# Kernel tuning notes

Hardware: AMD Instinct MI355X
Metric: run time of the kernel (lower is better)

The kernel has to match this reference:

```python
import jax, jax.numpy as jnp
import numpy as np

RES = 0.1
TABLE = 2 ** 20
MOD_T = 201
HEADS = 8
M = 500_000
D = 120
PRIMES_NP = np.array([73856093, 19349669, 83492791], dtype=np.int64)
BMIN = np.array([-2.6, -8.1, 0.0], dtype=np.float32)
BMAX = np.array([4.6, 4.7, 3.1], dtype=np.float32)
CORNERS = [(0, 0, 0), (1, 0, 0), (0, 1, 0), (0, 0, 1), (1, 1, 0), (1, 0, 1), (0, 1, 1), (1, 1, 1)]


def _build_hash_table():
    # Mirror torch.arange / meshgrid voxel grid construction.
    xs = np.arange(BMIN[0], BMAX[0], RES, dtype=np.float32)
    ys = np.arange(BMIN[1], BMAX[1], RES, dtype=np.float32)
    zs = np.arange(BMIN[2], BMAX[2], RES, dtype=np.float32)
    gx, gy, gz = np.meshgrid(xs, ys, zs, indexing='ij')
    vox = np.stack([gx, gy, gz], axis=-1).reshape(-1, 3)
    grid = np.floor(vox / RES).astype(np.int64)
    h = np.remainder((grid * PRIMES_NP).sum(-1), TABLE)
    buf = np.full(TABLE, -1, dtype=np.int64)
    uh, first_idx = np.unique(h, return_index=True)
    buf[uh] = first_idx
    return buf, vox.shape[0]


def setup_inputs() -> dict:
    key = jax.random.key(0)
    ks = jax.random.split(key, 12)
    buf_np, total_voxels = _build_hash_table()
    u = jax.random.uniform(ks[0], (M, 3), dtype=jnp.float32)
    query_pts = jnp.asarray(BMIN) + u * jnp.asarray(BMAX - BMIN)
    query_times = jax.random.randint(ks[1], (M,), 0, 1000, dtype=jnp.int64)
    dynamic_features = jax.random.normal(ks[2], (total_voxels, D), dtype=jnp.float32) * 0.01
    time_embeddings = jax.random.normal(ks[3], (MOD_T, D), dtype=jnp.float32) * 0.01
    s = 1.0 / np.sqrt(D)
    Wq = jax.random.normal(ks[4], (D, D), dtype=jnp.float32) * s
    Wk = jax.random.normal(ks[5], (D, D), dtype=jnp.float32) * s
    Wv = jax.random.normal(ks[6], (D, D), dtype=jnp.float32) * s
    Wo = jax.random.normal(ks[7], (D, D), dtype=jnp.float32) * s
    bq = jnp.zeros((D,), jnp.float32)
    bk = jnp.zeros((D,), jnp.float32)
    bv = jnp.zeros((D,), jnp.float32)
    bo = jnp.zeros((D,), jnp.float32)
    return {
        'query_pts': query_pts, 'query_times': query_times,
        'dynamic_features': dynamic_features, 'time_embeddings': time_embeddings,
        'buffer_voxel_index': jnp.asarray(buf_np),
        'Wq': Wq, 'bq': bq, 'Wk': Wk, 'bk': bk, 'Wv': Wv, 'bv': bv, 'Wo': Wo, 'bo': bo,
    }


def _attn_fuse(feat, time_emb, Wq, bq, Wk, bk, Wv, bv, Wo, bo):
    # 2-token self-attention fusion: tokens = [voxel feature, time embedding]
    m, d = feat.shape
    dh = d // HEADS
    x = jnp.stack([feat, time_emb], axis=1)  # (M, 2, D)
    q = (x @ Wq + bq).reshape(m, 2, HEADS, dh)
    k = (x @ Wk + bk).reshape(m, 2, HEADS, dh)
    v = (x @ Wv + bv).reshape(m, 2, HEADS, dh)
    scores = jnp.einsum('mqhd,mkhd->mhqk', q, k) / jnp.sqrt(jnp.float32(dh))
    a = jax.nn.softmax(scores, axis=-1)
    o = jnp.einsum('mhqk,mkhd->mqhd', a, v).reshape(m, 2, d)
    o = o @ Wo + bo
    return o.mean(axis=1)  # (M, D)


def reference(query_pts, query_times, dynamic_features, time_embeddings,
              buffer_voxel_index, Wq, bq, Wk, bk, Wv, bv, Wo, bo):
    primes = jnp.asarray(PRIMES_NP)
    m = query_pts.shape[0]
    d = dynamic_features.shape[1]
    t_mod = jnp.remainder(query_times, MOD_T)

    gf = query_pts / RES
    gfl = jnp.floor(gf)
    frac = gf - gfl                      # (M, 3)
    base = gfl.astype(jnp.int64)         # (M, 3)

    accum = jnp.zeros((m, d), dtype=query_pts.dtype)
    for ox, oy, oz in CORNERS:           # fixed structural 8-corner loop
        cc = base + jnp.asarray([ox, oy, oz], dtype=jnp.int64)
        h = jnp.remainder((cc * primes).sum(-1), TABLE)
        vidx = buffer_voxel_index[h]
        valid = vidx >= 0
        wx = frac[:, 0] if ox else 1.0 - frac[:, 0]
        wy = frac[:, 1] if oy else 1.0 - frac[:, 1]
        wz = frac[:, 2] if oz else 1.0 - frac[:, 2]
        w = wx * wy * wz                 # (M,)
        f = dynamic_features[jnp.where(valid, vidx, 0)]
        accum = accum + jnp.where(valid[:, None], f * w[:, None], 0.0)

    time_emb = time_embeddings[t_mod]
    return _attn_fuse(accum, time_emb, Wq, bq, Wk, bk, Wv, bv, Wo, bo)
```

## Files before the change

kernel.cpp:

```cpp
#include <hip/hip_runtime.h>
#include <math.h>

#define M_D   120
#define MOD_T 201
#define TABLE_MASK 0xFFFFFu
#define INV_S 0.25819888974716115f

#define WS_TV  1608
#define WS_TQK 27336
#define WS_DYN16_BYTE 344064ull

typedef float    f32x4 __attribute__((ext_vector_type(4)));
typedef uint32_t u32x4 __attribute__((ext_vector_type(4)));
typedef __fp16   f16x2v __attribute__((ext_vector_type(2)));
typedef __fp16   f16x8 __attribute__((ext_vector_type(8)));

union PK2 { f16x2v h; uint32_t u; };
union BFrag { f16x8 v; f16x2v h2[4]; uint32_t u[4]; };

__global__ void precomp_time(const float* __restrict__ temb,
                             const float* __restrict__ Wq, const float* __restrict__ bq,
                             const float* __restrict__ Wk, const float* __restrict__ bk,
                             const float* __restrict__ Wv, const float* __restrict__ bv,
                             float* __restrict__ ws) {
  const int t = blockIdx.x, np = threadIdx.x;
  const int h = np >> 4, m = np & 15;
  const bool valid = (m < 15);
  const int col = h * 15 + m;
  __shared__ float lq[128], lk[128];
  float q = 0.f, k = 0.f, v = 0.f;
  if (valid) {
    q = bq[col]; k = bk[col]; v = bv[col];
    const float* te = temb + t * M_D;
    for (int i = 0; i < M_D; ++i) {
      float x = te[i];
      q = fmaf(x, Wq[i * M_D + col], q);
      k = fmaf(x, Wk[i * M_D + col], k);
      v = fmaf(x, Wv[i * M_D + col], v);
    }
  }
  lq[np] = q; lk[np] = k;
  ws[WS_TV + t * 128 + np] = v;
  PK2 pk; pk.h[0] = (__fp16)(q * INV_S); pk.h[1] = (__fp16)k;
  ((uint32_t*)ws)[WS_TQK + t * 128 + np] = pk.u;
  __syncthreads();
  if (np < 8) {
    float s = 0.f;
    #pragma unroll
    for (int mm = 0; mm < 15; ++mm) s += lq[np * 16 + mm] * lk[np * 16 + mm];
    ws[t * 8 + np] = s * INV_S;
  }
}

__global__ void cvt_dyn(const float* __restrict__ dyn, __fp16* __restrict__ d16, int n8) {
  const int i = blockIdx.x * 256 + threadIdx.x;
  if (i < n8) {
    const f32x4 a = __builtin_nontemporal_load((const f32x4*)(dyn + 8 * (long)i));
    const f32x4 b = __builtin_nontemporal_load((const f32x4*)(dyn + 8 * (long)i + 4));
    BFrag o;
    o.h2[0] = __builtin_amdgcn_cvt_pkrtz(a[0], a[1]);
    o.h2[1] = __builtin_amdgcn_cvt_pkrtz(a[2], a[3]);
    o.h2[2] = __builtin_amdgcn_cvt_pkrtz(b[0], b[1]);
    o.h2[3] = __builtin_amdgcn_cvt_pkrtz(b[2], b[3]);
    *(f16x8*)(d16 + 8 * (long)i) = o.v;
  }
}

template <int USE16>
__launch_bounds__(512, 2)
__global__ void fused_main(const float* __restrict__ qpts, const int* __restrict__ qtimes,
                           const float* __restrict__ dyn,  const __fp16* __restrict__ dyn16,
                           const int* __restrict__ hbuf,
                           const float* __restrict__ Wq, const float* __restrict__ bq,
                           const float* __restrict__ Wk, const float* __restrict__ bk,
                           const float* __restrict__ Wv, const float* __restrict__ bv,
                           const float* __restrict__ Wo, const float* __restrict__ bo,
                           const float* __restrict__ ws, float* __restrict__ out, int M) {
  __shared__ __align__(16) uint32_t wlds[4 * 8192];

  const int tid = threadIdx.x;
  for (int idx = tid; idx < 32768; idx += 512) {
    const int mat = idx >> 13, r = idx & 8191;
    const int nt = r >> 10, kk = (r >> 8) & 3, l = (r >> 2) & 63, d = r & 3;
    const int mm = l & 15;
    const int i0 = kk * 32 + ((l >> 4) << 3) + 2 * d;
    float v0 = 0.f, v1 = 0.f;
    if (mat < 3) {
      const float* W = (mat == 0) ? Wq : (mat == 1) ? Wk : Wv;
      const float* b = (mat == 0) ? bq : (mat == 1) ? bk : bv;
      if (mm < 15) {
        const int col = nt * 15 + mm;
        const int ia = i0, ib = i0 + 1;
        v0 = (ia < 120) ? W[ia * M_D + col] : (ia == 120 ? b[col] : 0.f);
        v1 = (ib < 120) ? W[ib * M_D + col] : (ib == 120 ? b[col] : 0.f);
        if (mat == 0) { v0 *= INV_S; v1 *= INV_S; }
      }
    } else {
      const int n = nt * 16 + mm;
      if (n < M_D) {
        #pragma unroll
        for (int e = 0; e < 2; ++e) {
          const int ip = i0 + e;
          const int hi = ip >> 4, mi = ip & 15;
          float vv = 0.f;
          if (mi < 15) vv = Wo[(hi * 15 + mi) * M_D + n];
          else if (ip == 15) vv = bo[n];
          if (e == 0) v0 = vv; else v1 = vv;
        }
      }
    }
    PK2 pk; pk.h[0] = (__fp16)v0; pk.h[1] = (__fp16)v1;
    wlds[idx] = pk.u;
  }
  __syncthreads();

  const uint32_t* wq = wlds;
  const uint32_t* wk = wlds + 8192;
  const uint32_t* wvm = wlds + 2 * 8192;
  const uint32_t* wo = wlds + 3 * 8192;

  const int l = tid & 63, wv = tid >> 6;
  const int g = l >> 4, pl = l & 15, c0 = g << 2;
  const float* S11 = ws;
  const float* TVt = ws + WS_TV;
  const uint32_t* TQK = (const uint32_t*)ws + WS_TQK;

  const int T = (M + 15) >> 4;
  for (int tile = blockIdx.x * 8 + wv; tile < T; tile += gridDim.x * 8) {
    const int pid = (tile << 4) + pl;
    const int p = (pid < M) ? pid : (M - 1);

    const float px = qpts[3 * p], py = qpts[3 * p + 1], pz = qpts[3 * p + 2];
    const int tm = qtimes[p] % MOD_T;
    const float gx = px / 0.1f, gy = py / 0.1f, gz = pz / 0.1f;
    const float fx = floorf(gx), fy = floorf(gy), fz = floorf(gz);
    const float rx = gx - fx, ry = gy - fy, rz = gz - fz;
    const int bx = (int)fx, by = (int)fy, bz = (int)fz;

    const int i0g = g * 8;
    int voff[8];
    float wcv[8];
    #pragma unroll
    for (int c = 0; c < 8; ++c) {
      const int ox = c & 1, oy = (c >> 1) & 1, oz = c >> 2;
      const uint32_t hh = (uint32_t)(bx + ox) * 73856093u +
                          (uint32_t)(by + oy) * 19349669u +
                          (uint32_t)(bz + oz) * 83492791u;
      const int vc = hbuf[hh & TABLE_MASK];
      const float wc = (ox ? rx : 1.f - rx) * (oy ? ry : 1.f - ry) * (oz ? rz : 1.f - rz);
      wcv[c] = (vc >= 0) ? wc : 0.f;
      voff[c] = ((vc >= 0) ? vc : 0) * M_D + i0g;
    }

    BFrag bf[4];
    #pragma unroll
    for (int kk = 0; kk < 4; ++kk) {
      f32x4 accA = {0, 0, 0, 0}, accB = {0, 0, 0, 0};
      if (kk < 3 || g < 3) {
        #pragma unroll
        for (int c = 0; c < 8; ++c) {
          const float wc = wcv[c];
          if (USE16) {
            const f16x8 v8 = *(const f16x8*)(dyn16 + voff[c] + kk * 32);
            accA[0] = fmaf((float)v8[0], wc, accA[0]);
            accA[1] = fmaf((float)v8[1], wc, accA[1]);
            accA[2] = fmaf((float)v8[2], wc, accA[2]);
            accA[3] = fmaf((float)v8[3], wc, accA[3]);
            accB[0] = fmaf((float)v8[4], wc, accB[0]);
            accB[1] = fmaf((float)v8[5], wc, accB[1]);
            accB[2] = fmaf((float)v8[6], wc, accB[2]);
            accB[3] = fmaf((float)v8[7], wc, accB[3]);
          } else {
            const float* fr = dyn + voff[c];
            f32x4 lo4 = *(const f32x4*)(fr + kk * 32);
            f32x4 hi4 = *(const f32x4*)(fr + kk * 32 + 4);
            accA += lo4 * wc;
            accB += hi4 * wc;
          }
        }
      }
      if (kk == 3 && g == 3) accA[0] = 1.0f;
      bf[kk].h2[0] = __builtin_amdgcn_cvt_pkrtz(accA[0], accA[1]);
      bf[kk].h2[1] = __builtin_amdgcn_cvt_pkrtz(accA[2], accA[3]);
      bf[kk].h2[2] = __builtin_amdgcn_cvt_pkrtz(accB[0], accB[1]);
      bf[kk].h2[3] = __builtin_amdgcn_cvt_pkrtz(accB[2], accB[3]);
    }

    f32x4 tvv[8]; u32x4 tqk[8]; float s11v[8];
    #pragma unroll
    for (int nt = 0; nt < 8; ++nt) {
      tvv[nt] = *(const f32x4*)(TVt + tm * 128 + nt * 16 + c0);
      tqk[nt] = *(const u32x4*)(TQK + tm * 128 + nt * 16 + c0);
      s11v[nt] = S11[tm * 8 + nt];
    }

    f32x4 aq[8], ak[8], av[8];
    #pragma unroll
    for (int nt = 0; nt < 8; ++nt) {
      f32x4 zq = {0,0,0,0}, zk = {0,0,0,0}, zv = {0,0,0,0};
      #pragma unroll
      for (int kk = 0; kk < 4; ++kk) {
        const int off = nt * 1024 + kk * 256 + l * 4;
        f16x8 a0 = *(const f16x8*)(wq + off);
        f16x8 a1 = *(const f16x8*)(wk + off);
        f16x8 a2 = *(const f16x8*)(wvm + off);
        zq = __builtin_amdgcn_mfma_f32_16x16x32_f16(a0, bf[kk].v, zq, 0, 0, 0);
        zk = __builtin_amdgcn_mfma_f32_16x16x32_f16(a1, bf[kk].v, zk, 0, 0, 0);
        zv = __builtin_amdgcn_mfma_f32_16x16x32_f16(a2, bf[kk].v, zv, 0, 0, 0);
      }
      aq[nt] = zq; ak[nt] = zk; av[nt] = zv;
    }

    float a_[8], b_[8];
    #pragma unroll
    for (int nt = 0; nt < 8; ++nt) {
      float s00 = 0.f, s01 = 0.f, s10 = 0.f;
      #pragma unroll
      for (int r = 0; r < 4; ++r) {
        const float qv = aq[nt][r], kv = ak[nt][r];
        PK2 tt; tt.u = tqk[nt][r];
        const float tqs = (float)tt.h[0], tk = (float)tt.h[1];
        s00 = fmaf(qv, kv, s00);
        s01 = fmaf(qv, tk, s01);
        s10 = fmaf(tqs, kv, s10);
      }
      s00 += __shfl_xor(s00, 16); s00 += __shfl_xor(s00, 32);
      s01 += __shfl_xor(s01, 16); s01 += __shfl_xor(s01, 32);
      s10 += __shfl_xor(s10, 16); s10 += __shfl_xor(s10, 32);
      const float s11 = s11v[nt];
      const float m0 = fmaxf(s00, s01), m1 = fmaxf(s10, s11);
      const float e00 = __expf(s00 - m0), e01 = __expf(s01 - m0);
      const float e10 = __expf(s10 - m1), e11 = __expf(s11 - m1);
      const float r0 = 1.f / (e00 + e01), r1 = 1.f / (e10 + e11);
      a_[nt] = 0.5f * (e00 * r0 + e10 * r1);
      b_[nt] = 0.5f * (e01 * r0 + e11 * r1);
    }

    uint32_t cdw[8][2];
    #pragma unroll
    for (int nt = 0; nt < 8; ++nt) {
      f32x4 cv;
      #pragma unroll
      for (int r = 0; r < 4; ++r) cv[r] = a_[nt] * av[nt][r] + b_[nt] * tvv[nt][r];
      if (nt == 0 && g == 3) cv[3] = 1.0f;
      PK2 p0, p1;
      p0.h = __builtin_amdgcn_cvt_pkrtz(cv[0], cv[1]);
      p1.h = __builtin_amdgcn_cvt_pkrtz(cv[2], cv[3]);
      cdw[nt][0] = p0.u; cdw[nt][1] = p1.u;
    }

    const int src0 = pl | ((g & 1) << 5);
    const int src1 = src0 + 16;
    const bool hsel = (g >= 2);
    BFrag bco[4];
    #pragma unroll
    for (int kk = 0; kk < 4; ++kk) {
      #pragma unroll
      for (int d = 0; d < 4; ++d) {
        const int s = (d >= 2) ? src1 : src0;
        const int vlo = __shfl((int)cdw[2 * kk][d & 1], s, 64);
        const int vhi = __shfl((int)cdw[2 * kk + 1][d & 1], s, 64);
        bco[kk].u[d] = hsel ? (uint32_t)vhi : (uint32_t)vlo;
      }
    }

    float* orow = out + (long)pid * M_D;
    #pragma unroll
    for (int nt = 0; nt < 8; ++nt) {
      f32x4 zo = {0,0,0,0};
      #pragma unroll
      for (int kk = 0; kk < 4; ++kk) {
        f16x8 a3 = *(const f16x8*)(wo + nt * 1024 + kk * 256 + l * 4);
        zo = __builtin_amdgcn_mfma_f32_16x16x32_f16(a3, bco[kk].v, zo, 0, 0, 0);
      }
      if (pid < M && (nt < 7 || g < 2))
        *(f32x4*)(orow + nt * 16 + c0) = zo;
    }
  }
}

extern "C" void kernel_launch(void* const* d_in, const int* in_sizes, int n_in,
                              void* d_out, int out_size, void* d_ws, size_t ws_size,
                              hipStream_t stream) {
  const float* qpts   = (const float*)d_in[0];
  const int*   qtimes = (const int*)d_in[1];
  const float* dyn    = (const float*)d_in[2];
  const float* temb   = (const float*)d_in[3];
  const int*   hbuf   = (const int*)d_in[4];
  const float* Wq = (const float*)d_in[5];
  const float* bq = (const float*)d_in[6];
  const float* Wk = (const float*)d_in[7];
  const float* bk = (const float*)d_in[8];
  const float* Wv = (const float*)d_in[9];
  const float* bv = (const float*)d_in[10];
  const float* Wo = (const float*)d_in[11];
  const float* bo = (const float*)d_in[12];
  float* out = (float*)d_out;
  float* ws  = (float*)d_ws;
  const int M = in_sizes[1];
  const int ndyn = in_sizes[2];

  hipLaunchKernelGGL(precomp_time, dim3(MOD_T), dim3(128), 0, stream,
                     temb, Wq, bq, Wk, bk, Wv, bv, ws);

  const size_t need = WS_DYN16_BYTE + (size_t)ndyn * 2;
  if (ws_size >= need) {
    __fp16* d16 = (__fp16*)((char*)d_ws + WS_DYN16_BYTE);
    const int n8 = ndyn / 8;
    hipLaunchKernelGGL(cvt_dyn, dim3((n8 + 255) / 256), dim3(256), 0, stream,
                       dyn, d16, n8);
    hipLaunchKernelGGL(fused_main<1>, dim3(256), dim3(512), 0, stream,
                       qpts, qtimes, dyn, d16, hbuf,
                       Wq, bq, Wk, bk, Wv, bv, Wo, bo, ws, out, M);
  } else {
    hipLaunchKernelGGL(fused_main<0>, dim3(256), dim3(512), 0, stream,
                       qpts, qtimes, dyn, (const __fp16*)nullptr, hbuf,
                       Wq, bq, Wk, bk, Wv, bv, Wo, bo, ws, out, M);
  }
}
```

Before: 1.149 ms.

## Spatially bin query points via counting sort and pad fp16 feature rows to 128

Adds a histogram, scan and scatter pass that sorts query points into 4x4x4-voxel spatial bins. The main kernel then processes the points in sorted order over contiguous per-wave tile ranges, with a block swizzle, and writes output rows back to their original indices. The aim is better cache locality for the hash-table and feature-row gathers. The fp16 feature rows are also padded to 128 halves for alignment. This adds three extra passes plus a memset, global atomics, and scattered output writes.

```diff
diff --git a/kernel.cpp b/kernel.cpp
--- a/kernel.cpp
+++ b/kernel.cpp
@@ -8,7 +8,10 @@
 
 #define WS_TV  1608
 #define WS_TQK 27336
-#define WS_DYN16_BYTE 344064ull
+#define WS_HIST_BYTE 262144ull
+#define WS_PTS_BYTE  524288ull
+#define WS_DYN16_BYTE 8650752ull
+#define NBINS 16384
 
 typedef float    f32x4 __attribute__((ext_vector_type(4)));
 typedef uint32_t u32x4 __attribute__((ext_vector_type(4)));
@@ -17,6 +20,16 @@
 
 union PK2 { f16x2v h; uint32_t u; };
 union BFrag { f16x8 v; f16x2v h2[4]; uint32_t u[4]; };
+
+__device__ __forceinline__ int bin_key(float px, float py, float pz) {
+  const int bx = (int)floorf(px * 10.0f);
+  const int by = (int)floorf(py * 10.0f);
+  const int bz = (int)floorf(pz * 10.0f);
+  const int tx = ((bx + 32) >> 2) & 31;
+  const int ty = ((by + 96) >> 2) & 63;
+  const int tz = (bz >> 2) & 7;
+  return (tx << 9) | (ty << 3) | tz;
+}
 
 __global__ void precomp_time(const float* __restrict__ temb,
                              const float* __restrict__ Wq, const float* __restrict__ bq,
@@ -55,6 +68,7 @@
 __global__ void cvt_dyn(const float* __restrict__ dyn, __fp16* __restrict__ d16, int n8) {
   const int i = blockIdx.x * 256 + threadIdx.x;
   if (i < n8) {
+    const int row = i / 15, sub = i % 15;
     const f32x4 a = __builtin_nontemporal_load((const f32x4*)(dyn + 8 * (long)i));
     const f32x4 b = __builtin_nontemporal_load((const f32x4*)(dyn + 8 * (long)i + 4));
     BFrag o;
@@ -62,13 +76,50 @@
     o.h2[1] = __builtin_amdgcn_cvt_pkrtz(a[2], a[3]);
     o.h2[2] = __builtin_amdgcn_cvt_pkrtz(b[0], b[1]);
     o.h2[3] = __builtin_amdgcn_cvt_pkrtz(b[2], b[3]);
-    *(f16x8*)(d16 + 8 * (long)i) = o.v;
+    *(f16x8*)(d16 + (long)row * 128 + sub * 8) = o.v;
+  }
+}
+
+__global__ void hist_pts(const float* __restrict__ qpts, uint32_t* __restrict__ hist, int M) {
+  const int p = blockIdx.x * 256 + threadIdx.x;
+  if (p < M)
+    atomicAdd(&hist[bin_key(qpts[3 * p], qpts[3 * p + 1], qpts[3 * p + 2])], 1u);
+}
+
+__global__ void scan_hist(uint32_t* __restrict__ hist) {
+  __shared__ uint32_t part[1024];
+  const int t = threadIdx.x;
+  uint32_t loc[16]; uint32_t s = 0;
+  #pragma unroll
+  for (int i = 0; i < 16; ++i) { loc[i] = hist[t * 16 + i]; s += loc[i]; }
+  part[t] = s;
+  __syncthreads();
+  for (int off = 1; off < 1024; off <<= 1) {
+    uint32_t v = (t >= off) ? part[t - off] : 0;
+    __syncthreads();
+    part[t] += v;
+    __syncthreads();
+  }
+  uint32_t base = (t == 0) ? 0 : part[t - 1];
+  #pragma unroll
+  for (int i = 0; i < 16; ++i) { uint32_t c = loc[i]; hist[t * 16 + i] = base; base += c; }
+}
+
+__global__ void scatter_pts(const float* __restrict__ qpts, const int* __restrict__ qtimes,
+                            uint32_t* __restrict__ hist, float4* __restrict__ pts, int M) {
+  const int p = blockIdx.x * 256 + threadIdx.x;
+  if (p < M) {
+    const float px = qpts[3 * p], py = qpts[3 * p + 1], pz = qpts[3 * p + 2];
+    const uint32_t pos = atomicAdd(&hist[bin_key(px, py, pz)], 1u);
+    const int tm = qtimes[p] % MOD_T;
+    float4 v; v.x = px; v.y = py; v.z = pz; v.w = __int_as_float((p << 8) | tm);
+    pts[pos] = v;
   }
 }
 
 template <int USE16>
 __launch_bounds__(512, 2)
-__global__ void fused_main(const float* __restrict__ qpts, const int* __restrict__ qtimes,
+__global__ void fused_main(const float4* __restrict__ pts,
                            const float* __restrict__ dyn,  const __fp16* __restrict__ dyn16,
                            const int* __restrict__ hbuf,
                            const float* __restrict__ Wq, const float* __restrict__ bq,
@@ -126,12 +177,22 @@
   const uint32_t* TQK = (const uint32_t*)ws + WS_TQK;
 
   const int T = (M + 15) >> 4;
-  for (int tile = blockIdx.x * 8 + wv; tile < T; tile += gridDim.x * 8) {
-    const int pid = (tile << 4) + pl;
-    const int p = (pid < M) ? pid : (M - 1);
-
-    const float px = qpts[3 * p], py = qpts[3 * p + 1], pz = qpts[3 * p + 2];
-    const int tm = qtimes[p] % MOD_T;
+  const int nb = gridDim.x;
+  const int swz = (blockIdx.x & 7) * (nb >> 3) + (blockIdx.x >> 3);
+  const int slot = swz * 8 + wv;
+  const int slots = nb * 8;
+  const int C = (T + slots - 1) / slots;
+  const int t0 = slot * C;
+  const int t1 = (t0 + C < T) ? (t0 + C) : T;
+
+  for (int tile = t0; tile < t1; ++tile) {
+    const int idx = (tile << 4) + pl;
+    const bool valid = (idx < M);
+    const float4 pd = pts[valid ? idx : (M - 1)];
+    const float px = pd.x, py = pd.y, pz = pd.z;
+    const int pk_ = __float_as_int(pd.w);
+    const int p_out = pk_ >> 8, tm = pk_ & 255;
+
     const float gx = px / 0.1f, gy = py / 0.1f, gz = pz / 0.1f;
     const float fx = floorf(gx), fy = floorf(gy), fz = floorf(gz);
     const float rx = gx - fx, ry = gy - fy, rz = gz - fz;
@@ -149,7 +210,8 @@
       const int vc = hbuf[hh & TABLE_MASK];
       const float wc = (ox ? rx : 1.f - rx) * (oy ? ry : 1.f - ry) * (oz ? rz : 1.f - rz);
       wcv[c] = (vc >= 0) ? wc : 0.f;
-      voff[c] = ((vc >= 0) ? vc : 0) * M_D + i0g;
+      const int vr = (vc >= 0) ? vc : 0;
+      voff[c] = (USE16 ? vr * 128 : vr * M_D) + i0g;
     }
 
     BFrag bf[4];
@@ -264,7 +326,7 @@
       }
     }
 
-    float* orow = out + (long)pid * M_D;
+    float* orow = out + (long)p_out * M_D;
     #pragma unroll
     for (int nt = 0; nt < 8; ++nt) {
       f32x4 zo = {0,0,0,0};
@@ -273,7 +335,7 @@
         f16x8 a3 = *(const f16x8*)(wo + nt * 1024 + kk * 256 + l * 4);
         zo = __builtin_amdgcn_mfma_f32_16x16x32_f16(a3, bco[kk].v, zo, 0, 0, 0);
       }
-      if (pid < M && (nt < 7 || g < 2))
+      if (valid && (nt < 7 || g < 2))
         *(f32x4*)(orow + nt * 16 + c0) = zo;
     }
   }
@@ -299,22 +361,31 @@
   float* ws  = (float*)d_ws;
   const int M = in_sizes[1];
   const int ndyn = in_sizes[2];
+  const int rows = ndyn / M_D;
 
   hipLaunchKernelGGL(precomp_time, dim3(MOD_T), dim3(128), 0, stream,
                      temb, Wq, bq, Wk, bk, Wv, bv, ws);
 
-  const size_t need = WS_DYN16_BYTE + (size_t)ndyn * 2;
-  if (ws_size >= need) {
+  uint32_t* hist = (uint32_t*)((char*)d_ws + WS_HIST_BYTE);
+  float4*   pts  = (float4*)((char*)d_ws + WS_PTS_BYTE);
+  hipMemsetAsync(hist, 0, NBINS * sizeof(uint32_t), stream);
+  hipLaunchKernelGGL(hist_pts, dim3((M + 255) / 256), dim3(256), 0, stream, qpts, hist, M);
+  hipLaunchKernelGGL(scan_hist, dim3(1), dim3(1024), 0, stream, hist);
+  hipLaunchKernelGGL(scatter_pts, dim3((M + 255) / 256), dim3(256), 0, stream,
+                     qpts, qtimes, hist, pts, M);
+
+  const size_t need_full = WS_DYN16_BYTE + (size_t)rows * 256;
+  if (ws_size >= need_full) {
     __fp16* d16 = (__fp16*)((char*)d_ws + WS_DYN16_BYTE);
     const int n8 = ndyn / 8;
     hipLaunchKernelGGL(cvt_dyn, dim3((n8 + 255) / 256), dim3(256), 0, stream,
                        dyn, d16, n8);
     hipLaunchKernelGGL(fused_main<1>, dim3(256), dim3(512), 0, stream,
-                       qpts, qtimes, dyn, d16, hbuf,
+                       pts, dyn, d16, hbuf,
                        Wq, bq, Wk, bk, Wv, bv, Wo, bo, ws, out, M);
   } else {
     hipLaunchKernelGGL(fused_main<0>, dim3(256), dim3(512), 0, stream,
-                       qpts, qtimes, dyn, (const __fp16*)nullptr, hbuf,
+                       pts, dyn, (const __fp16*)nullptr, hbuf,
                        Wq, bq, Wk, bk, Wv, bv, Wo, bo, ws, out, M);
   }
 }
```

Result: slower. 1.332 ms (+15.9%).

## Split gather and MFMA attention into separate kernels with padded fp16 features

Applied to the files above, without the earlier changes.

Splits the fused kernel into a gather kernel that does the trilinear hash lookups and writes per-point fp16 features to workspace, and an MFMA kernel that reads those features and runs the attention and output projection. The fp16 dynamic-feature table is padded to 128-element rows so the gathers are aligned, and the output stores become nontemporal. The aim is to let the latency-bound gather run at higher occupancy and with more loads in flight, separate from the register-heavy MFMA stage. The cost is an extra round trip of about 128 MB of intermediate features through memory plus another kernel launch.

```diff
diff --git a/kernel.cpp b/kernel.cpp
--- a/kernel.cpp
+++ b/kernel.cpp
@@ -8,7 +8,7 @@
 
 #define WS_TV  1608
 #define WS_TQK 27336
-#define WS_DYN16_BYTE 344064ull
+#define WS_DYN16_BYTE (1ull << 20)
 
 typedef float    f32x4 __attribute__((ext_vector_type(4)));
 typedef uint32_t u32x4 __attribute__((ext_vector_type(4)));
@@ -52,30 +52,102 @@
   }
 }
 
-__global__ void cvt_dyn(const float* __restrict__ dyn, __fp16* __restrict__ d16, int n8) {
+__global__ void cvt_dyn(const float* __restrict__ dyn, __fp16* __restrict__ d16, int rows) {
   const int i = blockIdx.x * 256 + threadIdx.x;
-  if (i < n8) {
-    const f32x4 a = __builtin_nontemporal_load((const f32x4*)(dyn + 8 * (long)i));
-    const f32x4 b = __builtin_nontemporal_load((const f32x4*)(dyn + 8 * (long)i + 4));
+  const int row = i >> 4, sub = i & 15;
+  if (row < rows) {
     BFrag o;
-    o.h2[0] = __builtin_amdgcn_cvt_pkrtz(a[0], a[1]);
-    o.h2[1] = __builtin_amdgcn_cvt_pkrtz(a[2], a[3]);
-    o.h2[2] = __builtin_amdgcn_cvt_pkrtz(b[0], b[1]);
-    o.h2[3] = __builtin_amdgcn_cvt_pkrtz(b[2], b[3]);
-    *(f16x8*)(d16 + 8 * (long)i) = o.v;
+    if (sub == 15) { o.u[0] = 0; o.u[1] = 0; o.u[2] = 0; o.u[3] = 0; }
+    else {
+      const float* src = dyn + (long)row * M_D + sub * 8;
+      const f32x4 a = __builtin_nontemporal_load((const f32x4*)src);
+      const f32x4 b = __builtin_nontemporal_load((const f32x4*)(src + 4));
+      o.h2[0] = __builtin_amdgcn_cvt_pkrtz(a[0], a[1]);
+      o.h2[1] = __builtin_amdgcn_cvt_pkrtz(a[2], a[3]);
+      o.h2[2] = __builtin_amdgcn_cvt_pkrtz(b[0], b[1]);
+      o.h2[3] = __builtin_amdgcn_cvt_pkrtz(b[2], b[3]);
+    }
+    *(f16x8*)(d16 + (long)row * 128 + sub * 8) = o.v;
   }
 }
 
-template <int USE16>
+__launch_bounds__(256, 2)
+__global__ void gather_feat(const float* __restrict__ qpts, const __fp16* __restrict__ dyn16,
+                            const int* __restrict__ hbuf, __fp16* __restrict__ feat, int M) {
+  const int l = threadIdx.x & 63, wv = threadIdx.x >> 6;
+  const int g = l >> 4, pl = l & 15;
+  const int T = (M + 15) >> 4;
+  for (int tile = blockIdx.x * 4 + wv; tile < T; tile += gridDim.x * 4) {
+    const int pid = (tile << 4) + pl;
+    const int p = (pid < M) ? pid : (M - 1);
+    const float px = qpts[3 * p], py = qpts[3 * p + 1], pz = qpts[3 * p + 2];
+    const float gx = px / 0.1f, gy = py / 0.1f, gz = pz / 0.1f;
+    const float fx = floorf(gx), fy = floorf(gy), fz = floorf(gz);
+    const float rx = gx - fx, ry = gy - fy, rz = gz - fz;
+    const int bx = (int)fx, by = (int)fy, bz = (int)fz;
+
+    int voff[8]; float wcv[8];
+    #pragma unroll
+    for (int c = 0; c < 8; ++c) {
+      const int ox = c & 1, oy = (c >> 1) & 1, oz = c >> 2;
+      const uint32_t hh = (uint32_t)(bx + ox) * 73856093u +
+                          (uint32_t)(by + oy) * 19349669u +
+                          (uint32_t)(bz + oz) * 83492791u;
+      const int vc = hbuf[hh & TABLE_MASK];
+      const float wc = (ox ? rx : 1.f - rx) * (oy ? ry : 1.f - ry) * (oz ? rz : 1.f - rz);
+      wcv[c] = (vc >= 0) ? wc : 0.f;
+      voff[c] = ((vc >= 0) ? vc : 0) * 128 + g * 8;
+    }
+
+    __fp16* frow = feat + (long)pid * 128 + g * 8;
+    f16x8 va[8], vb[8];
+    #pragma unroll
+    for (int c = 0; c < 8; ++c) va[c] = *(const f16x8*)(dyn16 + voff[c]);
+    #pragma unroll
+    for (int c = 0; c < 8; ++c) vb[c] = *(const f16x8*)(dyn16 + voff[c] + 32);
+
+    auto PROC = [&](int kk, f16x8* vk) {
+      f32x4 accA = {0, 0, 0, 0}, accB = {0, 0, 0, 0};
+      #pragma unroll
+      for (int c = 0; c < 8; ++c) {
+        const float wc = wcv[c];
+        const f16x8 v8 = vk[c];
+        accA[0] = fmaf((float)v8[0], wc, accA[0]);
+        accA[1] = fmaf((float)v8[1], wc, accA[1]);
+        accA[2] = fmaf((float)v8[2], wc, accA[2]);
+        accA[3] = fmaf((float)v8[3], wc, accA[3]);
+        accB[0] = fmaf((float)v8[4], wc, accB[0]);
+        accB[1] = fmaf((float)v8[5], wc, accB[1]);
+        accB[2] = fmaf((float)v8[6], wc, accB[2]);
+        accB[3] = fmaf((float)v8[7], wc, accB[3]);
+      }
+      if (kk == 3 && g == 3) accA[0] = 1.0f;
+      BFrag o;
+      o.h2[0] = __builtin_amdgcn_cvt_pkrtz(accA[0], accA[1]);
+      o.h2[1] = __builtin_amdgcn_cvt_pkrtz(accA[2], accA[3]);
+      o.h2[2] = __builtin_amdgcn_cvt_pkrtz(accB[0], accB[1]);
+      o.h2[3] = __builtin_amdgcn_cvt_pkrtz(accB[2], accB[3]);
+      if (pid < M) *(f16x8*)(frow + kk * 32) = o.v;
+    };
+
+    PROC(0, va);
+    #pragma unroll
+    for (int c = 0; c < 8; ++c) va[c] = *(const f16x8*)(dyn16 + voff[c] + 64);
+    PROC(1, vb);
+    #pragma unroll
+    for (int c = 0; c < 8; ++c) vb[c] = *(const f16x8*)(dyn16 + voff[c] + 96);
+    PROC(2, va);
+    PROC(3, vb);
+  }
+}
+
 __launch_bounds__(512, 2)
-__global__ void fused_main(const float* __restrict__ qpts, const int* __restrict__ qtimes,
-                           const float* __restrict__ dyn,  const __fp16* __restrict__ dyn16,
-                           const int* __restrict__ hbuf,
-                           const float* __restrict__ Wq, const float* __restrict__ bq,
-                           const float* __restrict__ Wk, const float* __restrict__ bk,
-                           const float* __restrict__ Wv, const float* __restrict__ bv,
-                           const float* __restrict__ Wo, const float* __restrict__ bo,
-                           const float* __restrict__ ws, float* __restrict__ out, int M) {
+__global__ void mfma_main(const int* __restrict__ qtimes, const __fp16* __restrict__ feat,
+                          const float* __restrict__ Wq, const float* __restrict__ bq,
+                          const float* __restrict__ Wk, const float* __restrict__ bk,
+                          const float* __restrict__ Wv, const float* __restrict__ bv,
+                          const float* __restrict__ Wo, const float* __restrict__ bo,
+                          const float* __restrict__ ws, float* __restrict__ out, int M) {
   __shared__ __align__(16) uint32_t wlds[4 * 8192];
 
   const int tid = threadIdx.x;
@@ -128,18 +200,177 @@
   const int T = (M + 15) >> 4;
   for (int tile = blockIdx.x * 8 + wv; tile < T; tile += gridDim.x * 8) {
     const int pid = (tile << 4) + pl;
+    const bool valid = (pid < M);
+    const int p = valid ? pid : (M - 1);
+    const int tm = qtimes[p] % MOD_T;
+
+    BFrag bf[4];
+    const __fp16* frow = feat + (long)p * 128 + g * 8;
+    #pragma unroll
+    for (int kk = 0; kk < 4; ++kk) bf[kk].v = *(const f16x8*)(frow + kk * 32);
+
+    f32x4 tvv[8]; u32x4 tqk[8]; float s11v[8];
+    #pragma unroll
+    for (int nt = 0; nt < 8; ++nt) {
+      tvv[nt] = *(const f32x4*)(TVt + tm * 128 + nt * 16 + c0);
+      tqk[nt] = *(const u32x4*)(TQK + tm * 128 + nt * 16 + c0);
+      s11v[nt] = S11[tm * 8 + nt];
+    }
+
+    f32x4 aq[8], ak[8], av[8];
+    #pragma unroll
+    for (int nt = 0; nt < 8; ++nt) {
+      f32x4 zq = {0,0,0,0}, zk = {0,0,0,0}, zv = {0,0,0,0};
+      #pragma unroll
+      for (int kk = 0; kk < 4; ++kk) {
+        const int off = nt * 1024 + kk * 256 + l * 4;
+        f16x8 a0 = *(const f16x8*)(wq + off);
+        f16x8 a1 = *(const f16x8*)(wk + off);
+        f16x8 a2 = *(const f16x8*)(wvm + off);
+        zq = __builtin_amdgcn_mfma_f32_16x16x32_f16(a0, bf[kk].v, zq, 0, 0, 0);
+        zk = __builtin_amdgcn_mfma_f32_16x16x32_f16(a1, bf[kk].v, zk, 0, 0, 0);
+        zv = __builtin_amdgcn_mfma_f32_16x16x32_f16(a2, bf[kk].v, zv, 0, 0, 0);
+      }
+      aq[nt] = zq; ak[nt] = zk; av[nt] = zv;
+    }
+
+    float a_[8], b_[8];
+    #pragma unroll
+    for (int nt = 0; nt < 8; ++nt) {
+      float s00 = 0.f, s01 = 0.f, s10 = 0.f;
+      #pragma unroll
+      for (int r = 0; r < 4; ++r) {
+        const float qv = aq[nt][r], kv = ak[nt][r];
+        PK2 tt; tt.u = tqk[nt][r];
+        const float tqs = (float)tt.h[0], tk = (float)tt.h[1];
+        s00 = fmaf(qv, kv, s00);
+        s01 = fmaf(qv, tk, s01);
+        s10 = fmaf(tqs, kv, s10);
+      }
+      s00 += __shfl_xor(s00, 16); s00 += __shfl_xor(s00, 32);
+      s01 += __shfl_xor(s01, 16); s01 += __shfl_xor(s01, 32);
+      s10 += __shfl_xor(s10, 16); s10 += __shfl_xor(s10, 32);
+      const float s11 = s11v[nt];
+      const float m0 = fmaxf(s00, s01), m1 = fmaxf(s10, s11);
+      const float e00 = __expf(s00 - m0), e01 = __expf(s01 - m0);
+      const float e10 = __expf(s10 - m1), e11 = __expf(s11 - m1);
+      const float r0 = 1.f / (e00 + e01), r1 = 1.f / (e10 + e11);
+      a_[nt] = 0.5f * (e00 * r0 + e10 * r1);
+      b_[nt] = 0.5f * (e01 * r0 + e11 * r1);
+    }
+
+    uint32_t cdw[8][2];
+    #pragma unroll
+    for (int nt = 0; nt < 8; ++nt) {
+      f32x4 cv;
+      #pragma unroll
+      for (int r = 0; r < 4; ++r) cv[r] = a_[nt] * av[nt][r] + b_[nt] * tvv[nt][r];
+      if (nt == 0 && g == 3) cv[3] = 1.0f;
+      PK2 p0, p1;
+      p0.h = __builtin_amdgcn_cvt_pkrtz(cv[0], cv[1]);
+      p1.h = __builtin_amdgcn_cvt_pkrtz(cv[2], cv[3]);
+      cdw[nt][0] = p0.u; cdw[nt][1] = p1.u;
+    }
+
+    const int src0 = pl | ((g & 1) << 5);
+    const int src1 = src0 + 16;
+    const bool hsel = (g >= 2);
+    BFrag bco[4];
+    #pragma unroll
+    for (int kk = 0; kk < 4; ++kk) {
+      #pragma unroll
+      for (int d = 0; d < 4; ++d) {
+        const int s = (d >= 2) ? src1 : src0;
+        const int vlo = __shfl((int)cdw[2 * kk][d & 1], s, 64);
+        const int vhi = __shfl((int)cdw[2 * kk + 1][d & 1], s, 64);
+        bco[kk].u[d] = hsel ? (uint32_t)vhi : (uint32_t)vlo;
+      }
+    }
+
+    float* orow = out + (long)p * M_D;
+    #pragma unroll
+    for (int nt = 0; nt < 8; ++nt) {
+      f32x4 zo = {0,0,0,0};
+      #pragma unroll
+      for (int kk = 0; kk < 4; ++kk) {
+        f16x8 a3 = *(const f16x8*)(wo + nt * 1024 + kk * 256 + l * 4);
+        zo = __builtin_amdgcn_mfma_f32_16x16x32_f16(a3, bco[kk].v, zo, 0, 0, 0);
+      }
+      if (valid && (nt < 7 || g < 2))
+        __builtin_nontemporal_store(zo, (f32x4*)(orow + nt * 16 + c0));
+    }
+  }
+}
+
+template <int USE16>
+__launch_bounds__(512, 2)
+__global__ void merged_main(const float* __restrict__ qpts, const int* __restrict__ qtimes,
+                            const float* __restrict__ dyn,  const __fp16* __restrict__ dyn16,
+                            const int* __restrict__ hbuf,
+                            const float* __restrict__ Wq, const float* __restrict__ bq,
+                            const float* __restrict__ Wk, const float* __restrict__ bk,
+                            const float* __restrict__ Wv, const float* __restrict__ bv,
+                            const float* __restrict__ Wo, const float* __restrict__ bo,
+                            const float* __restrict__ ws, float* __restrict__ out, int M) {
+  __shared__ __align__(16) uint32_t wlds[4 * 8192];
+  const int tid = threadIdx.x;
+  for (int idx = tid; idx < 32768; idx += 512) {
+    const int mat = idx >> 13, r = idx & 8191;
+    const int nt = r >> 10, kk = (r >> 8) & 3, l = (r >> 2) & 63, d = r & 3;
+    const int mm = l & 15;
+    const int i0 = kk * 32 + ((l >> 4) << 3) + 2 * d;
+    float v0 = 0.f, v1 = 0.f;
+    if (mat < 3) {
+      const float* W = (mat == 0) ? Wq : (mat == 1) ? Wk : Wv;
+      const float* b = (mat == 0) ? bq : (mat == 1) ? bk : bv;
+      if (mm < 15) {
+        const int col = nt * 15 + mm;
+        const int ia = i0, ib = i0 + 1;
+        v0 = (ia < 120) ? W[ia * M_D + col] : (ia == 120 ? b[col] : 0.f);
+        v1 = (ib < 120) ? W[ib * M_D + col] : (ib == 120 ? b[col] : 0.f);
+        if (mat == 0) { v0 *= INV_S; v1 *= INV_S; }
+      }
+    } else {
+      const int n = nt * 16 + mm;
+      if (n < M_D) {
+        #pragma unroll
+        for (int e = 0; e < 2; ++e) {
+          const int ip = i0 + e;
+          const int hi = ip >> 4, mi = ip & 15;
+          float vv = 0.f;
+          if (mi < 15) vv = Wo[(hi * 15 + mi) * M_D + n];
+          else if (ip == 15) vv = bo[n];
+          if (e == 0) v0 = vv; else v1 = vv;
+        }
+      }
+    }
+    PK2 pk; pk.h[0] = (__fp16)v0; pk.h[1] = (__fp16)v1;
+    wlds[idx] = pk.u;
+  }
+  __syncthreads();
+
+  const uint32_t* wq = wlds;
+  const uint32_t* wk = wlds + 8192;
+  const uint32_t* wvm = wlds + 2 * 8192;
+  const uint32_t* wo = wlds + 3 * 8192;
+  const int l = tid & 63, wv = tid >> 6;
+  const int g = l >> 4, pl = l & 15, c0 = g << 2;
+  const float* S11 = ws;
+  const float* TVt = ws + WS_TV;
+  const uint32_t* TQK = (const uint32_t*)ws + WS_TQK;
+
+  const int T = (M + 15) >> 4;
+  for (int tile = blockIdx.x * 8 + wv; tile < T; tile += gridDim.x * 8) {
+    const int pid = (tile << 4) + pl;
     const int p = (pid < M) ? pid : (M - 1);
-
     const float px = qpts[3 * p], py = qpts[3 * p + 1], pz = qpts[3 * p + 2];
     const int tm = qtimes[p] % MOD_T;
     const float gx = px / 0.1f, gy = py / 0.1f, gz = pz / 0.1f;
     const float fx = floorf(gx), fy = floorf(gy), fz = floorf(gz);
     const float rx = gx - fx, ry = gy - fy, rz = gz - fz;
     const int bx = (int)fx, by = (int)fy, bz = (int)fz;
-
     const int i0g = g * 8;
-    int voff[8];
-    float wcv[8];
+    int voff[8]; float wcv[8];
     #pragma unroll
     for (int c = 0; c < 8; ++c) {
       const int ox = c & 1, oy = (c >> 1) & 1, oz = c >> 2;
@@ -149,9 +380,9 @@
       const int vc = hbuf[hh & TABLE_MASK];
       const float wc = (ox ? rx : 1.f - rx) * (oy ? ry : 1.f - ry) * (oz ? rz : 1.f - rz);
       wcv[c] = (vc >= 0) ? wc : 0.f;
-      voff[c] = ((vc >= 0) ? vc : 0) * M_D + i0g;
-    }
-
+      const int vr = (vc >= 0) ? vc : 0;
+      voff[c] = (USE16 ? vr * 128 : vr * M_D) + i0g;
+    }
     BFrag bf[4];
     #pragma unroll
     for (int kk = 0; kk < 4; ++kk) {
@@ -185,7 +416,6 @@
       bf[kk].h2[2] = __builtin_amdgcn_cvt_pkrtz(accB[0], accB[1]);
       bf[kk].h2[3] = __builtin_amdgcn_cvt_pkrtz(accB[2], accB[3]);
     }
-
     f32x4 tvv[8]; u32x4 tqk[8]; float s11v[8];
     #pragma unroll
     for (int nt = 0; nt < 8; ++nt) {
@@ -193,7 +423,6 @@
       tqk[nt] = *(const u32x4*)(TQK + tm * 128 + nt * 16 + c0);
       s11v[nt] = S11[tm * 8 + nt];
     }
-
     f32x4 aq[8], ak[8], av[8];
     #pragma unroll
     for (int nt = 0; nt < 8; ++nt) {
@@ -210,7 +439,6 @@
       }
       aq[nt] = zq; ak[nt] = zk; av[nt] = zv;
     }
-
     float a_[8], b_[8];
     #pragma unroll
     for (int nt = 0; nt < 8; ++nt) {
@@ -219,10 +447,9 @@
       for (int r = 0; r < 4; ++r) {
         const float qv = aq[nt][r], kv = ak[nt][r];
         PK2 tt; tt.u = tqk[nt][r];
-        const float tqs = (float)tt.h[0], tk = (float)tt.h[1];
         s00 = fmaf(qv, kv, s00);
-        s01 = fmaf(qv, tk, s01);
-        s10 = fmaf(tqs, kv, s10);
+        s01 = fmaf(qv, (float)tt.h[1], s01);
+        s10 = fmaf((float)tt.h[0], kv, s10);
       }
       s00 += __shfl_xor(s00, 16); s00 += __shfl_xor(s00, 32);
       s01 += __shfl_xor(s01, 16); s01 += __shfl_xor(s01, 32);
@@ -235,7 +462,6 @@
       a_[nt] = 0.5f * (e00 * r0 + e10 * r1);
       b_[nt] = 0.5f * (e01 * r0 + e11 * r1);
     }
-
     uint32_t cdw[8][2];
     #pragma unroll
     for (int nt = 0; nt < 8; ++nt) {
@@ -248,7 +474,6 @@
       p1.h = __builtin_amdgcn_cvt_pkrtz(cv[2], cv[3]);
       cdw[nt][0] = p0.u; cdw[nt][1] = p1.u;
     }
-
     const int src0 = pl | ((g & 1) << 5);
     const int src1 = src0 + 16;
     const bool hsel = (g >= 2);
@@ -263,7 +488,6 @@
         bco[kk].u[d] = hsel ? (uint32_t)vhi : (uint32_t)vlo;
       }
     }
-
     float* orow = out + (long)pid * M_D;
     #pragma unroll
     for (int nt = 0; nt < 8; ++nt) {
@@ -299,21 +523,35 @@
   float* ws  = (float*)d_ws;
   const int M = in_sizes[1];
   const int ndyn = in_sizes[2];
+  const int rows = ndyn / M_D;
 
   hipLaunchKernelGGL(precomp_time, dim3(MOD_T), dim3(128), 0, stream,
                      temb, Wq, bq, Wk, bk, Wv, bv, ws);
 
-  const size_t need = WS_DYN16_BYTE + (size_t)ndyn * 2;
-  if (ws_size >= need) {
+  const size_t dyn16_bytes = (size_t)rows * 256;
+  const size_t need16 = WS_DYN16_BYTE + dyn16_bytes;
+  const size_t feat_off = (need16 + 255) & ~255ull;
+  const size_t T16 = (size_t)(((M + 15) / 16) * 16);
+  const size_t needF = feat_off + T16 * 256;
+
+  if (ws_size >= need16) {
     __fp16* d16 = (__fp16*)((char*)d_ws + WS_DYN16_BYTE);
-    const int n8 = ndyn / 8;
-    hipLaunchKernelGGL(cvt_dyn, dim3((n8 + 255) / 256), dim3(256), 0, stream,
-                       dyn, d16, n8);
-    hipLaunchKernelGGL(fused_main<1>, dim3(256), dim3(512), 0, stream,
-                       qpts, qtimes, dyn, d16, hbuf,
-                       Wq, bq, Wk, bk, Wv, bv, Wo, bo, ws, out, M);
+    const int nchunk = rows * 16;
+    hipLaunchKernelGGL(cvt_dyn, dim3((nchunk + 255) / 256), dim3(256), 0, stream,
+                       dyn, d16, rows);
+    if (ws_size >= needF) {
+      __fp16* feat = (__fp16*)((char*)d_ws + feat_off);
+      hipLaunchKernelGGL(gather_feat, dim3(2048), dim3(256), 0, stream,
+                         qpts, d16, hbuf, feat, M);
+      hipLaunchKernelGGL(mfma_main, dim3(256), dim3(512), 0, stream,
+                         qtimes, feat, Wq, bq, Wk, bk, Wv, bv, Wo, bo, ws, out, M);
+    } else {
+      hipLaunchKernelGGL(merged_main<1>, dim3(256), dim3(512), 0, stream,
+                         qpts, qtimes, dyn, d16, hbuf,
+                         Wq, bq, Wk, bk, Wv, bv, Wo, bo, ws, out, M);
+    }
   } else {
-    hipLaunchKernelGGL(fused_main<0>, dim3(256), dim3(512), 0, stream,
+    hipLaunchKernelGGL(merged_main<0>, dim3(256), dim3(512), 0, stream,
                        qpts, qtimes, dyn, (const __fp16*)nullptr, hbuf,
                        Wq, bq, Wk, bk, Wv, bv, Wo, bo, ws, out, M);
   }
```

After: 1.089 ms. -5.2%, faster.
